# Optimization experiments

Hardware: AMD Instinct MI355X
Metric: run time of the kernel (lower is better)

The kernel has to match this reference:

```python
import jax, jax.numpy as jnp
import numpy as np

N, E, T, CIN, COUT = 20000, 160000, 8, 64, 128


def setup_inputs() -> dict:
    key = jax.random.key(0)
    ks = jax.random.split(key, 8)
    x = jax.random.normal(ks[0], (T, N, CIN), jnp.float32)
    edge_index = jax.random.randint(ks[1], (2, E), 0, N)
    edge_weight = jax.random.normal(ks[2], (E,), jnp.float32)
    # temporal Conv1d: kernel 3, xavier-ish small init (gain=0.1 in source)
    tconv_w = jax.random.normal(ks[3], (COUT, CIN, 3), jnp.float32) * 0.02
    tconv_b = jnp.zeros((COUT,), jnp.float32)
    ln_g = jnp.ones((COUT,), jnp.float32)
    ln_b = jnp.zeros((COUT,), jnp.float32)
    # residual 1x1 Conv1d (in != out channels)
    res_w = jax.random.normal(ks[4], (COUT, CIN), jnp.float32) * 0.05
    res_b = jnp.zeros((COUT,), jnp.float32)
    # GCNConv linear weight [out, in] and bias
    gcn_w = jax.random.normal(ks[5], (COUT, COUT), jnp.float32) * 0.05
    gcn_b = jnp.zeros((COUT,), jnp.float32)
    return dict(x=x, edge_index=edge_index, edge_weight=edge_weight,
                tconv_w=tconv_w, tconv_b=tconv_b, ln_g=ln_g, ln_b=ln_b,
                res_w=res_w, res_b=res_b, gcn_w=gcn_w, gcn_b=gcn_b)


def reference(x, edge_index, edge_weight, tconv_w, tconv_b, ln_g, ln_b,
              res_w, res_b, gcn_w, gcn_b):
    Tn, Nn, _ = x.shape
    xc = jnp.transpose(x, (1, 2, 0))  # [N, Cin, T]
    # temporal conv over T (kernel 3, pad 1)
    h = jax.lax.conv_general_dilated(
        xc, tconv_w, window_strides=(1,), padding=[(1, 1)],
        dimension_numbers=('NCH', 'OIH', 'NCH')) + tconv_b[None, :, None]
    h = jnp.transpose(h, (0, 2, 1))  # [N, T, Cout]
    # LayerNorm over channel dim
    mu = h.mean(-1, keepdims=True)
    var = ((h - mu) ** 2).mean(-1, keepdims=True)
    h = (h - mu) * jax.lax.rsqrt(var + 1e-5) * ln_g + ln_b
    h = jax.nn.relu(h)
    # 1x1 residual conv: [N,Cin,T] x [Cout,Cin] -> [N,T,Cout]
    res = jnp.einsum('nct,oc->nto', xc, res_w) + res_b
    xcmb = h + res  # [N, T, Cout]
    # --- GCNConv (PyG): softmax edge weights, self-loops, sym-normalize ---
    ew = jax.nn.softmax(edge_weight)  # softmax over all edges (dim=0)
    row, col = edge_index[0], edge_index[1]
    sl = jnp.arange(Nn)
    row_f = jnp.concatenate([row, sl])
    col_f = jnp.concatenate([col, sl])
    w_f = jnp.concatenate([ew, jnp.ones((Nn,), ew.dtype)])  # self-loop weight 1
    deg = jax.ops.segment_sum(w_f, col_f, num_segments=Nn)
    dinv = jnp.where(deg > 0, jax.lax.rsqrt(jnp.maximum(deg, 1e-12)), 0.0)
    norm = dinv[row_f] * w_f * dinv[col_f]  # [E+N]
    xt = jnp.einsum('ntc,oc->nto', xcmb, gcn_w)  # linear transform, all T at once
    msg = norm[:, None, None] * xt[row_f]        # gather sources: [E+N, T, Cout]
    agg = jax.ops.segment_sum(msg, col_f, num_segments=Nn) + gcn_b
    out = jax.nn.relu(agg)  # [N, T, Cout]
    return jnp.transpose(out, (1, 0, 2))  # [T, N, Cout] == stacked per-t list
```

## Files before the change

kernel.cpp:

```cpp
#include <hip/hip_runtime.h>
#include <math.h>

#define N_NODES 20000
#define E_EDGES 160000
#define T_STEPS 8
#define C_IN    64
#define C_OUT   128

typedef __bf16 bf16x8 __attribute__((ext_vector_type(8)));
typedef float  f32x4  __attribute__((ext_vector_type(4)));
#define MFMA16(a, b, c) __builtin_amdgcn_mfma_f32_16x16x32_bf16((a), (b), (c), 0, 0, 0)

__device__ __forceinline__ unsigned short f2u(float f) {
  __bf16 b = (__bf16)f;
  return __builtin_bit_cast(unsigned short, b);
}
__device__ __forceinline__ unsigned int pack2(float lo, float hi) {
  return (unsigned int)f2u(lo) | ((unsigned int)f2u(hi) << 16);
}

__device__ __forceinline__ float wredSum(float v) {
#pragma unroll
  for (int d = 32; d > 0; d >>= 1) v += __shfl_xor(v, d, 64);
  return v;
}
__device__ __forceinline__ float wredMax(float v) {
#pragma unroll
  for (int d = 32; d > 0; d >>= 1) v = fmaxf(v, __shfl_xor(v, d, 64));
  return v;
}
__device__ __forceinline__ int wredSumI(int v) {
#pragma unroll
  for (int d = 32; d > 0; d >>= 1) v += __shfl_xor(v, d, 64);
  return v;
}
__device__ __forceinline__ float bredSum(float v, float* sm4) {
  __syncthreads();
  v = wredSum(v);
  const int lane = threadIdx.x & 63, wid = threadIdx.x >> 6;
  if (lane == 0) sm4[wid] = v;
  __syncthreads();
  return sm4[0] + sm4[1] + sm4[2] + sm4[3];
}
__device__ __forceinline__ float bredMax(float v, float* sm4) {
  __syncthreads();
  v = wredMax(v);
  const int lane = threadIdx.x & 63, wid = threadIdx.x >> 6;
  if (lane == 0) sm4[wid] = v;
  __syncthreads();
  return fmaxf(fmaxf(sm4[0], sm4[1]), fmaxf(sm4[2], sm4[3]));
}
__device__ __forceinline__ int bredSumI(int v, int* sm4) {
  __syncthreads();
  v = wredSumI(v);
  const int lane = threadIdx.x & 63, wid = threadIdx.x >> 6;
  if (lane == 0) sm4[wid] = v;
  __syncthreads();
  return sm4[0] + sm4[1] + sm4[2] + sm4[3];
}

__global__ __launch_bounds__(256) void k_esoft(const float* __restrict__ w,
                                               float* __restrict__ pm, float* __restrict__ ps) {
  __shared__ float sm4[4];
  float m = -3.4e38f, s = 0.f;
  for (int i = blockIdx.x * 256 + threadIdx.x; i < E_EDGES; i += 256 * 256) {
    const float xw = w[i];
    if (xw > m) { s = s * expf(m - xw) + 1.f; m = xw; }
    else        { s += expf(xw - m); }
  }
  const float M = bredMax(m, sm4);
  const float sp = (s > 0.f) ? s * expf(m - M) : 0.f;
  const float S = bredSum(sp, sm4);
  if (threadIdx.x == 0) { pm[blockIdx.x] = M; ps[blockIdx.x] = S; }
}

__global__ __launch_bounds__(256) void k_edge(const float* __restrict__ w, const int* __restrict__ ei,
                                              const float* __restrict__ pm, const float* __restrict__ ps,
                                              float* __restrict__ ewv, float* __restrict__ deg,
                                              int* __restrict__ cnt) {
  __shared__ float sm4[4];
  const float mloc = pm[threadIdx.x];
  const float mx   = bredMax(mloc, sm4);
  const float sp   = ps[threadIdx.x] * expf(mloc - mx);
  const float sum  = bredSum(sp, sm4);
  const int e = blockIdx.x * 256 + threadIdx.x;
  const float v = expf(w[e] - mx) / sum;
  ewv[e] = v;
  const int c = ei[E_EDGES + e];
  atomicAdd(&deg[c], v);
  atomicAdd(&cnt[c], 1);
}

__global__ __launch_bounds__(256) void k_scanA(const int* __restrict__ cnt, const float* __restrict__ deg,
                                               float* __restrict__ dinv, int* __restrict__ csum) {
  __shared__ int sm4[4];
  const int i = blockIdx.x * 256 + threadIdx.x;
  const int v = (i < N_NODES) ? cnt[i] : 0;
  if (i < N_NODES) dinv[i] = rsqrtf(deg[i]);
  int s = wredSumI(v);
  const int lane = threadIdx.x & 63, wid = threadIdx.x >> 6;
  if (lane == 0) sm4[wid] = s;
  __syncthreads();
  if (threadIdx.x == 0) csum[blockIdx.x] = sm4[0] + sm4[1] + sm4[2] + sm4[3];
}

__global__ __launch_bounds__(256) void k_scanC(const int* __restrict__ cnt, const int* __restrict__ csum,
                                               int* __restrict__ off, int* __restrict__ cursor) {
  __shared__ int smI[4];
  __shared__ int wpart[4];
  const int tid = threadIdx.x, lane = tid & 63, wid = tid >> 6;
  const int nchunk = (N_NODES + 255) / 256;
  const int vb = (tid < nchunk && tid < blockIdx.x) ? csum[tid] : 0;
  const int base = bredSumI(vb, smI);
  const int i = blockIdx.x * 256 + tid;
  const int v = (i < N_NODES) ? cnt[i] : 0;
  int s = v;
#pragma unroll
  for (int d = 1; d < 64; d <<= 1) { const int u = __shfl_up(s, d, 64); if (lane >= d) s += u; }
  if (lane == 63) wpart[wid] = s;
  __syncthreads();
  int add = base;
#pragma unroll
  for (int wv = 0; wv < 4; ++wv) if (wv < wid) add += wpart[wv];
  if (i < N_NODES) { const int excl = add + (s - v); off[i] = excl; cursor[i] = excl; }
  if (i == N_NODES - 1) off[N_NODES] = E_EDGES;
}

__global__ __launch_bounds__(256) void k_norm_scatter(const int* __restrict__ ei, const float* __restrict__ ewv,
                                                      const float* __restrict__ dinv, int* __restrict__ cursor,
                                                      uint2* __restrict__ srcnrm) {
  const int e = blockIdx.x * 256 + threadIdx.x;
  const int r = ei[e], c = ei[E_EDGES + e];
  const float nm = dinv[r] * ewv[e] * dinv[c];
  const int pos = atomicAdd(&cursor[c], 1);
  srcnrm[pos] = make_uint2((unsigned int)r, __builtin_bit_cast(unsigned int, nm));
}

__global__ __launch_bounds__(256) void k_wprep(const float* __restrict__ tconv_w, const float* __restrict__ res_w,
                                               const float* __restrict__ gcn_w, unsigned int* __restrict__ Bf,
                                               float* __restrict__ deg, int* __restrict__ cnt) {
  const int gid = blockIdx.x * 256 + threadIdx.x;
  if (gid < N_NODES) { deg[gid] = 1.0f; cnt[gid] = 0; }
  float v0, v1;
  if (gid < 12288) {
    const int reg = gid & 3, l = (gid >> 2) & 63, ct = (gid >> 8) & 7, ks = gid >> 11;
    const int o = ct * 16 + (l & 15);
    const int k0 = ks * 32 + ((l >> 4) & 3) * 8 + reg * 2;
    const int c0 = k0 & 63, tap0 = k0 >> 6;
    const int c1 = (k0 + 1) & 63, tap1 = (k0 + 1) >> 6;
    v0 = tconv_w[o * 192 + c0 * 3 + tap0];
    v1 = tconv_w[o * 192 + c1 * 3 + tap1];
  } else if (gid < 16384) {
    const int g = gid - 12288;
    const int reg = g & 3, l = (g >> 2) & 63, ct = (g >> 8) & 7, ks = g >> 11;
    const int o = ct * 16 + (l & 15);
    const int k0 = ks * 32 + ((l >> 4) & 3) * 8 + reg * 2;
    v0 = res_w[o * 64 + k0];
    v1 = res_w[o * 64 + k0 + 1];
  } else {
    const int g = gid - 16384;
    const int reg = g & 3, l = (g >> 2) & 63, ct = (g >> 8) & 7, ks = g >> 11;
    const int o = ct * 16 + (l & 15);
    const int k0 = ks * 32 + ((l >> 4) & 3) * 8 + reg * 2;
    v0 = gcn_w[o * 128 + k0];
    v1 = gcn_w[o * 128 + k0 + 1];
  }
  Bf[gid] = pack2(v0, v1);
}

#define XS_NODE 720
#define XS_SLOT 72
#define AS2_STRIDE 136
__global__ __launch_bounds__(256, 2) void k_fuse(const float* __restrict__ x,
                                                 const float* __restrict__ tconv_b,
                                                 const float* __restrict__ ln_g, const float* __restrict__ ln_b,
                                                 const float* __restrict__ res_b,
                                                 const unsigned int* __restrict__ Bf,
                                                 unsigned char* __restrict__ xq,
                                                 float* __restrict__ qsc) {
  const int tid = threadIdx.x, lane = tid & 63, w = tid >> 6;
  const int l15 = lane & 15, lg = lane >> 4;
  const int n0 = blockIdx.x * 16;

  __shared__ __align__(16) unsigned short XsAs[128 * AS2_STRIDE];
  unsigned short* Xs  = XsAs;
  unsigned short* As2 = XsAs;
  __shared__ float psum[4][128], psq[4][128];
  __shared__ float smu[128], srs[128];
  __shared__ unsigned int nmax[16];

  if (tid < 16) nmax[tid] = 0u;

#pragma unroll
  for (int p = 0; p < 8; ++p) {
    const int chunk = p * 256 + tid;
    const int tq = chunk >> 8, nn = (chunk >> 4) & 15, c4 = chunk & 15;
    const float4 v = *(const float4*)(x + ((size_t)tq * N_NODES + n0 + nn) * C_IN + c4 * 4);
    uint2 pk; pk.x = pack2(v.x, v.y); pk.y = pack2(v.z, v.w);
    *(uint2*)&Xs[nn * XS_NODE + (tq + 1) * XS_SLOT + c4 * 4] = pk;
  }
#pragma unroll
  for (int p = 0; p < 3; ++p) {
    const int i = p * 256 + tid;
    if (i < 576) {
      const int nn = i / 36;
      const int r = i - nn * 36;
      const int sl = (r < 18) ? 0 : 9;
      const int of = ((r < 18) ? r : r - 18) * 4;
      *(uint2*)&Xs[nn * XS_NODE + sl * XS_SLOT + of] = make_uint2(0u, 0u);
    }
  }

  const uint4* Bf4 = (const uint4*)Bf;
  uint4 Bc[2][6], Br[2][2];
#pragma unroll
  for (int ct = 0; ct < 2; ++ct) {
    const int ctg = w * 2 + ct;
#pragma unroll
    for (int ks = 0; ks < 6; ++ks) Bc[ct][ks] = Bf4[(ks * 8 + ctg) * 64 + lane];
#pragma unroll
    for (int ks = 0; ks < 2; ++ks) Br[ct][ks] = Bf4[3072 + (ks * 8 + ctg) * 64 + lane];
  }
  float cb[2], rb[2], gv[2], bv[2];
#pragma unroll
  for (int ct = 0; ct < 2; ++ct) {
    const int col = w * 32 + ct * 16 + l15;
    cb[ct] = tconv_b[col]; rb[ct] = res_b[col]; gv[ct] = ln_g[col]; bv[ct] = ln_b[col];
  }
  __syncthreads();

  f32x4 accC[8][2], accR[8][2];
#pragma unroll
  for (int rt = 0; rt < 8; ++rt)
#pragma unroll
    for (int ct = 0; ct < 2; ++ct) { accC[rt][ct] = (f32x4)0.f; accR[rt][ct] = (f32x4)0.f; }

#pragma unroll
  for (int ks = 0; ks < 6; ++ks) {
    bf16x8 af[8];
    const int slot = (l15 & 7) + (ks >> 1);
    const int koff = slot * XS_SLOT + (ks & 1) * 32 + lg * 8;
#pragma unroll
    for (int rt = 0; rt < 8; ++rt) {
      const int node = rt * 2 + (l15 >> 3);
      af[rt] = *(const bf16x8*)&Xs[node * XS_NODE + koff];
    }
#pragma unroll
    for (int rt = 0; rt < 8; ++rt)
#pragma unroll
      for (int ct = 0; ct < 2; ++ct)
        accC[rt][ct] = MFMA16(af[rt], __builtin_bit_cast(bf16x8, Bc[ct][ks]), accC[rt][ct]);
    if (ks == 2 || ks == 3) {
#pragma unroll
      for (int rt = 0; rt < 8; ++rt)
#pragma unroll
        for (int ct = 0; ct < 2; ++ct)
          accR[rt][ct] = MFMA16(af[rt], __builtin_bit_cast(bf16x8, Br[ct][ks - 2]), accR[rt][ct]);
    }
  }

#pragma unroll
  for (int rt = 0; rt < 8; ++rt) {
    float s[4], s2[4];
#pragma unroll
    for (int j = 0; j < 4; ++j) {
      const float h0 = accC[rt][0][j] + cb[0];
      const float h1 = accC[rt][1][j] + cb[1];
      accC[rt][0][j] = h0; accC[rt][1][j] = h1;
      s[j] = h0 + h1; s2[j] = h0 * h0 + h1 * h1;
    }
#pragma unroll
    for (int d = 1; d < 16; d <<= 1)
#pragma unroll
      for (int j = 0; j < 4; ++j) { s[j] += __shfl_xor(s[j], d, 64); s2[j] += __shfl_xor(s2[j], d, 64); }
    if (l15 == 0)
#pragma unroll
      for (int j = 0; j < 4; ++j) {
        psum[w][rt * 16 + lg * 4 + j] = s[j];
        psq[w][rt * 16 + lg * 4 + j] = s2[j];
      }
  }
  __syncthreads();
  if (tid < 128) {
    const float S  = psum[0][tid] + psum[1][tid] + psum[2][tid] + psum[3][tid];
    const float S2 = psq[0][tid] + psq[1][tid] + psq[2][tid] + psq[3][tid];
    const float mu = S * (1.f / 128.f);
    const float var = S2 * (1.f / 128.f) - mu * mu;
    smu[tid] = mu; srs[tid] = rsqrtf(var + 1e-5f);
  }
  __syncthreads();

#pragma unroll
  for (int rt = 0; rt < 8; ++rt)
#pragma unroll
    for (int j = 0; j < 4; ++j) {
      const int row = rt * 16 + lg * 4 + j;
      const float mu = smu[row], rs = srs[row];
      const int sw = ((row >> 3) & 1) << 4;
#pragma unroll
      for (int ct = 0; ct < 2; ++ct) {
        float xc = (accC[rt][ct][j] - mu) * rs * gv[ct] + bv[ct];
        xc = fmaxf(xc, 0.f) + accR[rt][ct][j] + rb[ct];
        const int col = w * 32 + ct * 16 + l15;
        As2[row * AS2_STRIDE + (col ^ sw)] = f2u(xc);
      }
    }
  __syncthreads();

  uint4 Bg[2][4];
#pragma unroll
  for (int ct = 0; ct < 2; ++ct)
#pragma unroll
    for (int ks = 0; ks < 4; ++ks) Bg[ct][ks] = Bf4[4096 + (ks * 8 + (w * 2 + ct)) * 64 + lane];

  f32x4 acc[8][2];
#pragma unroll
  for (int rt = 0; rt < 8; ++rt)
#pragma unroll
    for (int ct = 0; ct < 2; ++ct) acc[rt][ct] = (f32x4)0.f;

  const int swr = ((l15 >> 3) & 1) << 4;
#pragma unroll
  for (int ks = 0; ks < 4; ++ks) {
    bf16x8 af[8];
    const int koff = (ks * 32 + lg * 8) ^ swr;
#pragma unroll
    for (int rt = 0; rt < 8; ++rt)
      af[rt] = *(const bf16x8*)&As2[(rt * 16 + l15) * AS2_STRIDE + koff];
#pragma unroll
    for (int rt = 0; rt < 8; ++rt)
#pragma unroll
      for (int ct = 0; ct < 2; ++ct)
        acc[rt][ct] = MFMA16(af[rt], __builtin_bit_cast(bf16x8, Bg[ct][ks]), acc[rt][ct]);
  }

#pragma unroll
  for (int rt = 0; rt < 8; ++rt) {
    const int nn = rt * 2 + (lg >> 1);
    float m = 0.f;
#pragma unroll
    for (int ct = 0; ct < 2; ++ct)
#pragma unroll
      for (int j = 0; j < 4; ++j) m = fmaxf(m, fabsf(acc[rt][ct][j]));
    atomicMax(&nmax[nn], __builtin_bit_cast(unsigned int, m));
  }
  __syncthreads();
  if (tid < 16) qsc[n0 + tid] = __builtin_bit_cast(float, nmax[tid]) * (1.f / 127.f);

  const int t0 = (lg & 1) * 4;
#pragma unroll
  for (int rt = 0; rt < 8; ++rt) {
    const int nn = rt * 2 + (lg >> 1);
    const size_t n = (size_t)(n0 + nn);
    const float mx = __builtin_bit_cast(float, nmax[nn]);
    const float inv = (mx > 0.f) ? 127.f / mx : 0.f;
#pragma unroll
    for (int ct = 0; ct < 2; ++ct) {
      const int col = w * 32 + ct * 16 + l15;
      unsigned int pk8 = 0;
#pragma unroll
      for (int j = 0; j < 4; ++j) {
        const int q = (int)rintf(acc[rt][ct][j] * inv) + 128;
        pk8 |= ((unsigned int)q) << (8 * j);
      }
      *(unsigned int*)(xq + (n * C_OUT + col) * T_STEPS + t0) = pk8;
    }
  }
}

__global__ __launch_bounds__(256) void k_agg(const unsigned char* __restrict__ xq,
                                             const float* __restrict__ qsc,
                                             const uint2* __restrict__ srcnrm,
                                             const int* __restrict__ off, const float* __restrict__ dinv,
                                             const float* __restrict__ gcn_b, float* __restrict__ out) {
  const int tid = threadIdx.x, lane = tid & 63, w = tid >> 6;
  const int j = blockIdx.x * 4 + w;
  const int s = off[j], e = off[j + 1];
  const float d2 = dinv[j] * dinv[j];

  float acc[2][8];
#pragma unroll
  for (int h = 0; h < 2; ++h)
#pragma unroll
    for (int t = 0; t < 8; ++t) acc[h][t] = 0.f;

  float summul;
  {
    const float mul = d2 * qsc[j];
    summul = mul;
    const uint2 qa = *(const uint2*)(xq + ((size_t)j * C_OUT + lane) * T_STEPS);
    const uint2 qb = *(const uint2*)(xq + ((size_t)j * C_OUT + 64 + lane) * T_STEPS);
#pragma unroll
    for (int tt = 0; tt < 4; ++tt) {
      acc[0][tt]     = fmaf((float)((qa.x >> (8 * tt)) & 0xffu), mul, acc[0][tt]);
      acc[0][4 + tt] = fmaf((float)((qa.y >> (8 * tt)) & 0xffu), mul, acc[0][4 + tt]);
      acc[1][tt]     = fmaf((float)((qb.x >> (8 * tt)) & 0xffu), mul, acc[1][tt]);
      acc[1][4 + tt] = fmaf((float)((qb.y >> (8 * tt)) & 0xffu), mul, acc[1][4 + tt]);
    }
  }

  for (int k = s; k < e; ++k) {
    const uint2 sn = srcnrm[k];
    const int r = (int)sn.x;
    const float mul = __builtin_bit_cast(float, sn.y) * qsc[r];
    summul += mul;
    const uint2 qa = *(const uint2*)(xq + ((size_t)r * C_OUT + lane) * T_STEPS);
    const uint2 qb = *(const uint2*)(xq + ((size_t)r * C_OUT + 64 + lane) * T_STEPS);
#pragma unroll
    for (int tt = 0; tt < 4; ++tt) {
      acc[0][tt]     = fmaf((float)((qa.x >> (8 * tt)) & 0xffu), mul, acc[0][tt]);
      acc[0][4 + tt] = fmaf((float)((qa.y >> (8 * tt)) & 0xffu), mul, acc[0][4 + tt]);
      acc[1][tt]     = fmaf((float)((qb.x >> (8 * tt)) & 0xffu), mul, acc[1][tt]);
      acc[1][4 + tt] = fmaf((float)((qb.y >> (8 * tt)) & 0xffu), mul, acc[1][4 + tt]);
    }
  }

  const float corr = 128.f * summul;
  const float b0 = gcn_b[lane], b1 = gcn_b[64 + lane];
#pragma unroll
  for (int h = 0; h < 2; ++h) {
    const float bo = h ? b1 : b0;
#pragma unroll
    for (int t = 0; t < 8; ++t) {
      const float v = acc[h][t] - corr + bo;
      out[((size_t)t * N_NODES + j) * C_OUT + h * 64 + lane] = fmaxf(v, 0.f);
    }
  }
}

extern "C" void kernel_launch(void* const* d_in, const int* in_sizes, int n_in,
                              void* d_out, int out_size, void* d_ws, size_t ws_size,
                              hipStream_t stream) {
  (void)in_sizes; (void)n_in; (void)out_size; (void)ws_size;
  const float* x       = (const float*)d_in[0];
  const int*   ei      = (const int*)d_in[1];
  const float* ewt     = (const float*)d_in[2];
  const float* tconv_w = (const float*)d_in[3];
  const float* tconv_b = (const float*)d_in[4];
  const float* ln_g    = (const float*)d_in[5];
  const float* ln_b    = (const float*)d_in[6];
  const float* res_w   = (const float*)d_in[7];
  const float* res_b   = (const float*)d_in[8];
  const float* gcn_w   = (const float*)d_in[9];
  const float* gcn_b   = (const float*)d_in[10];
  float* out = (float*)d_out;

  unsigned char* xq = (unsigned char*)d_ws;
  float* qsc  = (float*)(xq + (size_t)N_NODES * C_OUT * T_STEPS);
  unsigned int* Bf = (unsigned int*)(qsc + N_NODES);
  float* ewv   = (float*)(Bf + 24576);
  float* deg   = ewv + E_EDGES;
  float* dinv  = deg + N_NODES;
  float* pm    = dinv + N_NODES;
  float* ps    = pm + 256;
  int*   cnt    = (int*)(ps + 256);
  int*   off    = cnt + N_NODES;
  int*   cursor = off + N_NODES + 1;
  int*   csum   = cursor + N_NODES;
  uint2* srcnrm = (uint2*)(((size_t)(csum + 128) + 15) & ~(size_t)15);

  const int nblk = (N_NODES + 255) / 256;
  const int eblk = E_EDGES / 256;

  k_wprep<<<96, 256, 0, stream>>>(tconv_w, res_w, gcn_w, Bf, deg, cnt);
  k_esoft<<<256, 256, 0, stream>>>(ewt, pm, ps);
  k_edge<<<eblk, 256, 0, stream>>>(ewt, ei, pm, ps, ewv, deg, cnt);
  k_scanA<<<nblk, 256, 0, stream>>>(cnt, deg, dinv, csum);
  k_scanC<<<nblk, 256, 0, stream>>>(cnt, csum, off, cursor);
  k_norm_scatter<<<eblk, 256, 0, stream>>>(ei, ewv, dinv, cursor, srcnrm);

  k_fuse<<<1250, 256, 0, stream>>>(x, tconv_b, ln_g, ln_b, res_b, Bf, xq, qsc);
  k_agg<<<N_NODES / 4, 256, 0, stream>>>(xq, qsc, srcnrm, off, dinv, gcn_b, out);
}
```

Measured before the change: 135.6 us.

## Merge scan kernels, fold quant scale into edge norms, batch edge-list loads

Replaces the two-pass scan (block partials, then offsets) with a single kernel where each block re-sums all preceding counts directly, which removes one launch. Moves the edge normalize-and-scatter after the fused feature kernel so the per-source quantization scale can be folded into the stored edge multiplier, removing a dependent gather from the aggregation loop. The aggregation loop now loads 64 edge entries per wave in one coalesced read and broadcasts them with shuffles instead of issuing a scalar load per edge. The merged scan does redundant reads of the count array that grow with block index.

```diff
diff --git a/kernel.cpp b/kernel.cpp
--- a/kernel.cpp
+++ b/kernel.cpp
@@ -91,28 +91,18 @@
   atomicAdd(&cnt[c], 1);
 }
 
-__global__ __launch_bounds__(256) void k_scanA(const int* __restrict__ cnt, const float* __restrict__ deg,
-                                               float* __restrict__ dinv, int* __restrict__ csum) {
-  __shared__ int sm4[4];
-  const int i = blockIdx.x * 256 + threadIdx.x;
-  const int v = (i < N_NODES) ? cnt[i] : 0;
-  if (i < N_NODES) dinv[i] = rsqrtf(deg[i]);
-  int s = wredSumI(v);
-  const int lane = threadIdx.x & 63, wid = threadIdx.x >> 6;
-  if (lane == 0) sm4[wid] = s;
-  __syncthreads();
-  if (threadIdx.x == 0) csum[blockIdx.x] = sm4[0] + sm4[1] + sm4[2] + sm4[3];
-}
-
-__global__ __launch_bounds__(256) void k_scanC(const int* __restrict__ cnt, const int* __restrict__ csum,
-                                               int* __restrict__ off, int* __restrict__ cursor) {
+__global__ __launch_bounds__(256) void k_scan2(const int* __restrict__ cnt, const float* __restrict__ deg,
+                                               float* __restrict__ dinv, int* __restrict__ off,
+                                               int* __restrict__ cursor) {
   __shared__ int smI[4];
   __shared__ int wpart[4];
   const int tid = threadIdx.x, lane = tid & 63, wid = tid >> 6;
-  const int nchunk = (N_NODES + 255) / 256;
-  const int vb = (tid < nchunk && tid < blockIdx.x) ? csum[tid] : 0;
-  const int base = bredSumI(vb, smI);
   const int i = blockIdx.x * 256 + tid;
+  if (i < N_NODES) dinv[i] = rsqrtf(deg[i]);
+  int part = 0;
+  const int lim = blockIdx.x * 256;
+  for (int j = tid; j < lim; j += 256) part += cnt[j];
+  const int base = bredSumI(part, smI);
   const int v = (i < N_NODES) ? cnt[i] : 0;
   int s = v;
 #pragma unroll
@@ -127,13 +117,13 @@
 }
 
 __global__ __launch_bounds__(256) void k_norm_scatter(const int* __restrict__ ei, const float* __restrict__ ewv,
-                                                      const float* __restrict__ dinv, int* __restrict__ cursor,
-                                                      uint2* __restrict__ srcnrm) {
+                                                      const float* __restrict__ dinv, const float* __restrict__ qsc,
+                                                      int* __restrict__ cursor, uint2* __restrict__ srcnrm) {
   const int e = blockIdx.x * 256 + threadIdx.x;
   const int r = ei[e], c = ei[E_EDGES + e];
-  const float nm = dinv[r] * ewv[e] * dinv[c];
+  const float mul = dinv[r] * ewv[e] * dinv[c] * qsc[r];
   const int pos = atomicAdd(&cursor[c], 1);
-  srcnrm[pos] = make_uint2((unsigned int)r, __builtin_bit_cast(unsigned int, nm));
+  srcnrm[pos] = make_uint2((unsigned int)r, __builtin_bit_cast(unsigned int, mul));
 }
 
 __global__ __launch_bounds__(256) void k_wprep(const float* __restrict__ tconv_w, const float* __restrict__ res_w,
@@ -399,19 +389,24 @@
     }
   }
 
-  for (int k = s; k < e; ++k) {
-    const uint2 sn = srcnrm[k];
-    const int r = (int)sn.x;
-    const float mul = __builtin_bit_cast(float, sn.y) * qsc[r];
-    summul += mul;
-    const uint2 qa = *(const uint2*)(xq + ((size_t)r * C_OUT + lane) * T_STEPS);
-    const uint2 qb = *(const uint2*)(xq + ((size_t)r * C_OUT + 64 + lane) * T_STEPS);
-#pragma unroll
-    for (int tt = 0; tt < 4; ++tt) {
-      acc[0][tt]     = fmaf((float)((qa.x >> (8 * tt)) & 0xffu), mul, acc[0][tt]);
-      acc[0][4 + tt] = fmaf((float)((qa.y >> (8 * tt)) & 0xffu), mul, acc[0][4 + tt]);
-      acc[1][tt]     = fmaf((float)((qb.x >> (8 * tt)) & 0xffu), mul, acc[1][tt]);
-      acc[1][4 + tt] = fmaf((float)((qb.y >> (8 * tt)) & 0xffu), mul, acc[1][4 + tt]);
+  for (int cs = s; cs < e; cs += 64) {
+    const uint2 sn = srcnrm[cs + lane];
+    const int   rv = (int)sn.x;
+    const float mv = __builtin_bit_cast(float, sn.y);
+    const int cnt = min(64, e - cs);
+    for (int k = 0; k < cnt; ++k) {
+      const int   r   = __shfl(rv, k, 64);
+      const float mul = __shfl(mv, k, 64);
+      summul += mul;
+      const uint2 qa = *(const uint2*)(xq + ((size_t)r * C_OUT + lane) * T_STEPS);
+      const uint2 qb = *(const uint2*)(xq + ((size_t)r * C_OUT + 64 + lane) * T_STEPS);
+#pragma unroll
+      for (int tt = 0; tt < 4; ++tt) {
+        acc[0][tt]     = fmaf((float)((qa.x >> (8 * tt)) & 0xffu), mul, acc[0][tt]);
+        acc[0][4 + tt] = fmaf((float)((qa.y >> (8 * tt)) & 0xffu), mul, acc[0][4 + tt]);
+        acc[1][tt]     = fmaf((float)((qb.x >> (8 * tt)) & 0xffu), mul, acc[1][tt]);
+        acc[1][4 + tt] = fmaf((float)((qb.y >> (8 * tt)) & 0xffu), mul, acc[1][4 + tt]);
+      }
     }
   }
 
@@ -456,8 +451,7 @@
   int*   cnt    = (int*)(ps + 256);
   int*   off    = cnt + N_NODES;
   int*   cursor = off + N_NODES + 1;
-  int*   csum   = cursor + N_NODES;
-  uint2* srcnrm = (uint2*)(((size_t)(csum + 128) + 15) & ~(size_t)15);
+  uint2* srcnrm = (uint2*)(((size_t)(cursor + N_NODES) + 15) & ~(size_t)15);
 
   const int nblk = (N_NODES + 255) / 256;
   const int eblk = E_EDGES / 256;
@@ -465,10 +459,8 @@
   k_wprep<<<96, 256, 0, stream>>>(tconv_w, res_w, gcn_w, Bf, deg, cnt);
   k_esoft<<<256, 256, 0, stream>>>(ewt, pm, ps);
   k_edge<<<eblk, 256, 0, stream>>>(ewt, ei, pm, ps, ewv, deg, cnt);
-  k_scanA<<<nblk, 256, 0, stream>>>(cnt, deg, dinv, csum);
-  k_scanC<<<nblk, 256, 0, stream>>>(cnt, csum, off, cursor);
-  k_norm_scatter<<<eblk, 256, 0, stream>>>(ei, ewv, dinv, cursor, srcnrm);
-
+  k_scan2<<<nblk, 256, 0, stream>>>(cnt, deg, dinv, off, cursor);
   k_fuse<<<1250, 256, 0, stream>>>(x, tconv_b, ln_g, ln_b, res_b, Bf, xq, qsc);
+  k_norm_scatter<<<eblk, 256, 0, stream>>>(ei, ewv, dinv, qsc, cursor, srcnrm);
   k_agg<<<N_NODES / 4, 256, 0, stream>>>(xq, qsc, srcnrm, off, dinv, gcn_b, out);
 }
```

Result: slower. 142.5 us (+5.1%).
